# Performance work log

Hardware: AMD Instinct MI355X
Metric: run time of the kernel (lower is better)

Reference implementation:

```python
import jax, jax.numpy as jnp
import numpy as np

B, S, DIM = 2, 2048, 1024
HID = 2048          # multiple_of-rounded hidden dim
E, NSH, TOPK = 8, 2, 2


def _ffn(x, w1, w2, w3):
    return (jax.nn.silu(x @ w1.T) * (x @ w3.T)) @ w2.T


def setup_inputs() -> dict:
    key = jax.random.key(0)
    ks = jax.random.split(key, 8)
    sc = 0.02  # init scale for stability
    return {
        "x": jax.random.normal(ks[0], (B, S, DIM), jnp.float32),
        "router_w": jax.random.normal(ks[1], (E, DIM), jnp.float32) * sc,
        "expert_bias": jnp.zeros((E,), jnp.float32),
        "w1": jax.random.normal(ks[2], (E, HID, DIM), jnp.float32) * sc,
        "w3": jax.random.normal(ks[3], (E, HID, DIM), jnp.float32) * sc,
        "w2": jax.random.normal(ks[4], (E, DIM, HID), jnp.float32) * sc,
        "sw1": jax.random.normal(ks[5], (NSH, HID, DIM), jnp.float32) * sc,
        "sw3": jax.random.normal(ks[6], (NSH, HID, DIM), jnp.float32) * sc,
        "sw2": jax.random.normal(ks[7], (NSH, DIM, HID), jnp.float32) * sc,
    }


def reference(x, router_w, expert_bias, w1, w3, w2, sw1, sw3, sw2):
    bs, sl, d = x.shape
    xf = x.reshape(-1, d)  # [T, d]

    # shared experts (always-on)
    shared = jnp.zeros_like(xf)
    for i in range(sw1.shape[0]):
        shared = shared + _ffn(xf, sw1[i], sw2[i], sw3[i])

    # router with aux-free load-balance bias
    logits = xf @ router_w.T + expert_bias  # [T, E]
    rw, sel = jax.lax.top_k(logits, TOPK)   # [T, K]
    rw = jax.nn.softmax(rw.astype(jnp.float32), axis=-1).astype(x.dtype)

    # combine weights per (token, expert): sum of routing weights over topk slots
    onehot = jax.nn.one_hot(sel, E, dtype=x.dtype)        # [T, K, E]
    combine = jnp.einsum('tk,tke->te', rw, onehot)        # [T, E]

    # per-expert FFN accumulated via scan (equivalent to gather-FFN-scatter)
    def body(acc, ew):
        e1, e3, e2, cw = ew  # cw: [T]
        acc = acc + cw[:, None] * _ffn(xf, e1, e2, e3)
        return acc, None

    out, _ = jax.lax.scan(body, jnp.zeros_like(xf), (w1, w3, w2, combine.T))
    out = out + shared
    return out.reshape(bs, sl, -1)
```

## Files before the change

### kernel.cpp

```cpp
#include <hip/hip_runtime.h>
#include <stdint.h>

#define T_TOK 4096
#define DIMD  1024
#define HIDN  2048
#define NEXP  8
#define RMAX  9216

typedef float f32x4 __attribute__((ext_vector_type(4)));
typedef short s16x8 __attribute__((ext_vector_type(8)));

__device__ __forceinline__ uint16_t f2bf(float f) {
    uint32_t u = __builtin_bit_cast(uint32_t, f);
    u += 0x7fffu + ((u >> 16) & 1u);
    return (uint16_t)(u >> 16);
}
__device__ __forceinline__ float bf2f(uint32_t h) {
    return __builtin_bit_cast(float, h << 16);
}
__device__ __forceinline__ uint32_t pk2(float a, float b) {
    return (uint32_t)f2bf(a) | ((uint32_t)f2bf(b) << 16);
}
__device__ __forceinline__ int swz(int r, int cbyte) {
    return r * 128 + (cbyte ^ ((r & 7) << 4));
}
__device__ __forceinline__ void gload16(const void* g, void* l) {
    __builtin_amdgcn_global_load_lds(
        (const __attribute__((address_space(1))) void*)g,
        (__attribute__((address_space(3))) void*)l, 16, 0, 0);
}
__device__ __forceinline__ void stage128x64(const uint16_t* gbase, int ldk,
                                            char* lds, int wv, int lane) {
    #pragma unroll
    for (int i = 0; i < 4; ++i) {
        int s = (wv * 4 + i) * 64 + lane;
        int row = s >> 3;
        int cb = ((s & 7) << 4) ^ ((row & 7) << 4);
        gload16(gbase + (size_t)row * ldk + (cb >> 1), lds + ((wv * 4 + i) << 10));
    }
}


__global__ void cvt_x_kernel(const float* __restrict__ x, uint16_t* __restrict__ xb) {
    int i = blockIdx.x * blockDim.x + threadIdx.x;
    float4 v = ((const float4*)x)[i];
    uint2 o; o.x = pk2(v.x, v.y); o.y = pk2(v.z, v.w);
    ((uint2*)xb)[i] = o;
}

__global__ void cvt_w_kernel(const float* __restrict__ s, uint16_t* __restrict__ d, int nquads) {
    int i = blockIdx.x * blockDim.x + threadIdx.x;
    int stride = gridDim.x * blockDim.x;
    for (; i < nquads; i += stride) {
        float4 v = ((const float4*)s)[i];
        uint2 o; o.x = pk2(v.x, v.y); o.y = pk2(v.z, v.w);
        ((uint2*)d)[i] = o;
    }
}

__global__ void router_kernel(const float* __restrict__ x, const float* __restrict__ rw,
                              const float* __restrict__ bias,
                              int* __restrict__ sel, float* __restrict__ wgt) {
    int t = blockIdx.x;
    int lane = threadIdx.x;
    int e = lane & 7, seg = lane >> 3;
    const float* xr = x + (size_t)t * DIMD + seg * 128;
    const float* wr = rw + (size_t)e * DIMD + seg * 128;
    float s = 0.f;
    #pragma unroll 8
    for (int i = 0; i < 128; ++i) s += xr[i] * wr[i];
    s += __shfl_xor(s, 8, 64);
    s += __shfl_xor(s, 16, 64);
    s += __shfl_xor(s, 32, 64);
    __shared__ float lg[8];
    if (lane < 8) lg[lane] = s + bias[lane];
    __syncthreads();
    if (lane == 0) {
        float l0 = -1e30f; int i0 = 0;
        #pragma unroll
        for (int i = 0; i < 8; ++i) { float v = lg[i]; if (v > l0) { l0 = v; i0 = i; } }
        float l1 = -1e30f; int i1 = 0;
        #pragma unroll
        for (int i = 0; i < 8; ++i) { if (i == i0) continue; float v = lg[i]; if (v > l1) { l1 = v; i1 = i; } }
        float e1 = expf(l1 - l0);
        float d = 1.f + e1;
        sel[t * 2] = i0; sel[t * 2 + 1] = i1;
        wgt[t * 2] = 1.f / d; wgt[t * 2 + 1] = e1 / d;
    }
}

__global__ void count_kernel(const int* __restrict__ sel, int* __restrict__ cnt) {
    int i = blockIdx.x * blockDim.x + threadIdx.x;
    if (i < T_TOK * 2) atomicAdd(&cnt[sel[i]], 1);
}

__global__ void offs_kernel(const int* __restrict__ cnt, int* __restrict__ offs) {
    if (threadIdx.x == 0 && blockIdx.x == 0) {
        int o = 0;
        for (int e = 0; e < NEXP; ++e) { offs[e] = o; o += (cnt[e] + 127) & ~127; }
        offs[NEXP] = o;
    }
}

__global__ void assign_kernel(const int* __restrict__ sel, const int* __restrict__ offs,
                              int* __restrict__ fill, int* __restrict__ row_of) {
    int i = blockIdx.x * blockDim.x + threadIdx.x;
    if (i < T_TOK * 2) {
        int e = sel[i];
        row_of[i] = offs[e] + atomicAdd(&fill[e], 1);
    }
}

__global__ void gather_kernel(const uint16_t* __restrict__ xb, const int* __restrict__ row_of,
                              uint16_t* __restrict__ Xg) {
    int slot = blockIdx.x;
    int pos = row_of[slot];
    int t = slot >> 1;
    const uint4* src = (const uint4*)(xb + (size_t)t * DIMD);
    uint4* dst = (uint4*)(Xg + (size_t)pos * DIMD);
    dst[threadIdx.x] = src[threadIdx.x];
}

__global__ void combine_kernel(const uint16_t* __restrict__ H2g, const int* __restrict__ row_of,
                               const float* __restrict__ wgt, float* __restrict__ out) {
    int t = blockIdx.x;
    int c = threadIdx.x * 8;
    int r0 = row_of[t * 2], r1 = row_of[t * 2 + 1];
    float w0 = wgt[t * 2], w1 = wgt[t * 2 + 1];
    uint4 a = *(const uint4*)(H2g + (size_t)r0 * DIMD + c);
    uint4 b = *(const uint4*)(H2g + (size_t)r1 * DIMD + c);
    float* o = out + (size_t)t * DIMD + c;
    o[0] += w0 * bf2f(a.x & 0xffffu) + w1 * bf2f(b.x & 0xffffu);
    o[1] += w0 * bf2f(a.x >> 16)     + w1 * bf2f(b.x >> 16);
    o[2] += w0 * bf2f(a.y & 0xffffu) + w1 * bf2f(b.y & 0xffffu);
    o[3] += w0 * bf2f(a.y >> 16)     + w1 * bf2f(b.y >> 16);
    o[4] += w0 * bf2f(a.z & 0xffffu) + w1 * bf2f(b.z & 0xffffu);
    o[5] += w0 * bf2f(a.z >> 16)     + w1 * bf2f(b.z >> 16);
    o[6] += w0 * bf2f(a.w & 0xffffu) + w1 * bf2f(b.w & 0xffffu);
    o[7] += w0 * bf2f(a.w >> 16)     + w1 * bf2f(b.w >> 16);
}


template<int ROUTED>
__global__ __launch_bounds__(256, 2)
void gemm13_kernel(const uint16_t* __restrict__ A,
                   const uint16_t* __restrict__ W1, const uint16_t* __restrict__ W3,
                   uint16_t* __restrict__ H, int ldh,
                   const int* __restrict__ offs) {
    __shared__ __align__(16) char lds[49152];
    char* As  = lds;
    char* B1s = lds + 16384;
    char* B3s = lds + 32768;

    const int K = DIMD;
    int row0 = blockIdx.x * 128;
    const uint16_t *b1 = W1, *b3 = W3;
    if (ROUTED) {
        if (row0 >= offs[NEXP]) return;
        int e = 0;
        while (row0 >= offs[e + 1]) ++e;
        size_t eo = (size_t)e * HIDN * DIMD;
        b1 += eo; b3 += eo;
    }
    int col0 = blockIdx.y * 128;

    int tid = threadIdx.x, lane = tid & 63;
    int wv = tid >> 6, wm = wv >> 1, wn = wv & 1;

    f32x4 acc1[4][4] = {};
    f32x4 acc3[4][4] = {};

    for (int kt = 0; kt < K; kt += 64) {
        __syncthreads();
        stage128x64(A  + (size_t)row0 * K + kt, K, As,  wv, lane);
        stage128x64(b1 + (size_t)col0 * K + kt, K, B1s, wv, lane);
        stage128x64(b3 + (size_t)col0 * K + kt, K, B3s, wv, lane);
        __syncthreads();

        #pragma unroll
        for (int s = 0; s < 2; ++s) {
            int cb = s * 64 + ((lane >> 4) << 4);
            s16x8 av[4];
            #pragma unroll
            for (int i = 0; i < 4; ++i)
                av[i] = *(const s16x8*)(As + swz(wm * 64 + i * 16 + (lane & 15), cb));
            #pragma unroll
            for (int j = 0; j < 4; ++j) {
                int br = wn * 64 + j * 16 + (lane & 15);
                s16x8 bv1 = *(const s16x8*)(B1s + swz(br, cb));
                s16x8 bv3 = *(const s16x8*)(B3s + swz(br, cb));
                #pragma unroll
                for (int i = 0; i < 4; ++i) {
                    acc1[i][j] = __builtin_amdgcn_mfma_f32_16x16x32_bf16(av[i], bv1, acc1[i][j], 0, 0, 0);
                    acc3[i][j] = __builtin_amdgcn_mfma_f32_16x16x32_bf16(av[i], bv3, acc3[i][j], 0, 0, 0);
                }
            }
        }
    }

    #pragma unroll
    for (int i = 0; i < 4; ++i) {
        #pragma unroll
        for (int j = 0; j < 4; ++j) {
            #pragma unroll
            for (int rg = 0; rg < 4; ++rg) {
                int row = row0 + wm * 64 + i * 16 + ((lane >> 4) << 2) + rg;
                int col = col0 + wn * 64 + j * 16 + (lane & 15);
                float a1 = acc1[i][j][rg];
                float a3 = acc3[i][j][rg];
                float hv = (a1 / (1.f + __expf(-a1))) * a3;
                H[(size_t)row * ldh + col] = f2bf(hv);
            }
        }
    }
}

template<int ROUTED>
__global__ __launch_bounds__(256, 3)
void gemm2_kernel(const uint16_t* __restrict__ A, int lda,
                  const uint16_t* __restrict__ W2, void* __restrict__ Cout,
                  const int* __restrict__ offs,
                  int K, int kSplit, long long expStride) {
    __shared__ __align__(16) char lds[32768];
    char* As = lds;
    char* Bs = lds + 16384;

    int row0 = blockIdx.x * 128;
    const uint16_t* b2 = W2;
    if (ROUTED) {
        if (row0 >= offs[NEXP]) return;
        int e = 0;
        while (row0 >= offs[e + 1]) ++e;
        b2 += (size_t)e * DIMD * HIDN;
    }
    int col0 = blockIdx.y * 128;

    int tid = threadIdx.x, lane = tid & 63;
    int wv = tid >> 6, wm = wv >> 1, wn = wv & 1;

    f32x4 acc[4][4] = {};

    for (int kt = 0; kt < K; kt += 64) {
        const uint16_t* bb = b2 + (size_t)(kt / kSplit) * expStride + (kt % kSplit);
        __syncthreads();
        stage128x64(A  + (size_t)row0 * lda + kt, lda, As, wv, lane);
        stage128x64(bb + (size_t)col0 * kSplit, kSplit, Bs, wv, lane);
        __syncthreads();

        #pragma unroll
        for (int s = 0; s < 2; ++s) {
            int cb = s * 64 + ((lane >> 4) << 4);
            s16x8 av[4];
            #pragma unroll
            for (int i = 0; i < 4; ++i)
                av[i] = *(const s16x8*)(As + swz(wm * 64 + i * 16 + (lane & 15), cb));
            #pragma unroll
            for (int j = 0; j < 4; ++j) {
                s16x8 bv = *(const s16x8*)(Bs + swz(wn * 64 + j * 16 + (lane & 15), cb));
                #pragma unroll
                for (int i = 0; i < 4; ++i)
                    acc[i][j] = __builtin_amdgcn_mfma_f32_16x16x32_bf16(av[i], bv, acc[i][j], 0, 0, 0);
            }
        }
    }

    #pragma unroll
    for (int i = 0; i < 4; ++i) {
        #pragma unroll
        for (int j = 0; j < 4; ++j) {
            #pragma unroll
            for (int rg = 0; rg < 4; ++rg) {
                int row = row0 + wm * 64 + i * 16 + ((lane >> 4) << 2) + rg;
                int col = col0 + wn * 64 + j * 16 + (lane & 15);
                float v = acc[i][j][rg];
                if (ROUTED) ((uint16_t*)Cout)[(size_t)row * DIMD + col] = f2bf(v);
                else        ((float*)Cout)[(size_t)row * DIMD + col] += v;
            }
        }
    }
}


extern "C" void kernel_launch(void* const* d_in, const int* in_sizes, int n_in,
                              void* d_out, int out_size, void* d_ws, size_t ws_size,
                              hipStream_t stream) {
    const float* x   = (const float*)d_in[0];
    const float* rw  = (const float*)d_in[1];
    const float* eb  = (const float*)d_in[2];
    const float* w1  = (const float*)d_in[3];
    const float* w3  = (const float*)d_in[4];
    const float* w2  = (const float*)d_in[5];
    const float* sw1 = (const float*)d_in[6];
    const float* sw3 = (const float*)d_in[7];
    const float* sw2 = (const float*)d_in[8];
    float* out = (float*)d_out;

    const int EW = NEXP * HIDN * DIMD;
    const int SW = 2 * HIDN * DIMD;

    char* ws = (char*)d_ws;
    size_t off = 0;
    auto alloc = [&](size_t b) { char* p = ws + off; off = (off + b + 255) & ~(size_t)255; return p; };
    uint16_t* xb  = (uint16_t*)alloc((size_t)T_TOK * DIMD * 2);
    uint16_t* Xg  = (uint16_t*)alloc((size_t)RMAX * DIMD * 2);
    uint16_t* Hg  = (uint16_t*)alloc((size_t)RMAX * HIDN * 2);
    uint16_t* H2g = (uint16_t*)alloc((size_t)RMAX * DIMD * 2);
    uint16_t* w1b = (uint16_t*)alloc((size_t)EW * 2);
    uint16_t* w3b = (uint16_t*)alloc((size_t)EW * 2);
    uint16_t* w2b = (uint16_t*)alloc((size_t)EW * 2);
    uint16_t* sw1b = (uint16_t*)alloc((size_t)SW * 2);
    uint16_t* sw3b = (uint16_t*)alloc((size_t)SW * 2);
    uint16_t* sw2b = (uint16_t*)alloc((size_t)SW * 2);
    int*   sel    = (int*)  alloc(T_TOK * 2 * 4);
    float* wgt    = (float*)alloc(T_TOK * 2 * 4);
    int*   row_of = (int*)  alloc(T_TOK * 2 * 4);
    int*   cnt    = (int*)  alloc(64);
    int*   fill   = (int*)  alloc(64);
    int*   offs   = (int*)  alloc(64);

    hipMemsetAsync(cnt, 0, 64, stream);
    hipMemsetAsync(fill, 0, 64, stream);
    hipMemsetAsync(Xg, 0, (size_t)RMAX * DIMD * 2, stream);
    hipMemsetAsync(out, 0, (size_t)out_size * sizeof(float), stream);

    cvt_w_kernel<<<2048, 256, 0, stream>>>(w1,  w1b,  EW / 4);
    cvt_w_kernel<<<2048, 256, 0, stream>>>(w3,  w3b,  EW / 4);
    cvt_w_kernel<<<2048, 256, 0, stream>>>(w2,  w2b,  EW / 4);
    cvt_w_kernel<<<1024, 256, 0, stream>>>(sw1, sw1b, SW / 4);
    cvt_w_kernel<<<1024, 256, 0, stream>>>(sw3, sw3b, SW / 4);
    cvt_w_kernel<<<1024, 256, 0, stream>>>(sw2, sw2b, SW / 4);

    cvt_x_kernel<<<4096, 256, 0, stream>>>(x, xb);
    router_kernel<<<T_TOK, 64, 0, stream>>>(x, rw, eb, sel, wgt);
    count_kernel<<<32, 256, 0, stream>>>(sel, cnt);
    offs_kernel<<<1, 1, 0, stream>>>(cnt, offs);
    assign_kernel<<<32, 256, 0, stream>>>(sel, offs, fill, row_of);
    gather_kernel<<<T_TOK * 2, 128, 0, stream>>>(xb, row_of, Xg);

    gemm13_kernel<1><<<dim3(RMAX / 128, HIDN / 128), 256, 0, stream>>>(Xg, w1b, w3b, Hg, HIDN, offs);
    gemm2_kernel<1><<<dim3(RMAX / 128, DIMD / 128), 256, 0, stream>>>(Hg, HIDN, w2b, (void*)H2g, offs,
                                                                      HIDN, HIDN, 0);
    combine_kernel<<<T_TOK, 128, 0, stream>>>(H2g, row_of, wgt, out);

    gemm13_kernel<0><<<dim3(T_TOK / 128, (2 * HIDN) / 128), 256, 0, stream>>>(xb, sw1b, sw3b, Hg, 2 * HIDN, nullptr);
    gemm2_kernel<0><<<dim3(T_TOK / 128, DIMD / 128), 256, 0, stream>>>(Hg, 2 * HIDN, sw2b, (void*)out, nullptr,
                                                                       2 * HIDN, HIDN, (long long)DIMD * HIDN);
}
```

Baseline: 503.4 us.

## Merge conversion kernels, swap GEMM grid axes, raise gemm13 occupancy bound

Replaces the seven separate fp32-to-bf16 conversion launches with a single kernel that walks all seven segments. This removes several launches and their tail effects. The GEMM grids are transposed so blockIdx.x walks output columns, meaning consecutive blocks share the same A row-tile, which should improve L2 reuse of activations and of the per-expert weights. gemm13's launch bound is raised from 2 to 3 blocks per CU, which may force register spilling given its two 4x4 accumulator sets.

```diff
diff --git a/kernel.cpp b/kernel.cpp
--- a/kernel.cpp
+++ b/kernel.cpp
@@ -41,20 +41,25 @@
 }
 
 
-__global__ void cvt_x_kernel(const float* __restrict__ x, uint16_t* __restrict__ xb) {
-    int i = blockIdx.x * blockDim.x + threadIdx.x;
-    float4 v = ((const float4*)x)[i];
-    uint2 o; o.x = pk2(v.x, v.y); o.y = pk2(v.z, v.w);
-    ((uint2*)xb)[i] = o;
-}
-
-__global__ void cvt_w_kernel(const float* __restrict__ s, uint16_t* __restrict__ d, int nquads) {
-    int i = blockIdx.x * blockDim.x + threadIdx.x;
+struct CvtArgs {
+    const float* s[7];
+    uint16_t*    d[7];
+    int          nq[7];
+};
+
+__global__ void cvt_all_kernel(CvtArgs a) {
+    int base = blockIdx.x * blockDim.x + threadIdx.x;
     int stride = gridDim.x * blockDim.x;
-    for (; i < nquads; i += stride) {
-        float4 v = ((const float4*)s)[i];
-        uint2 o; o.x = pk2(v.x, v.y); o.y = pk2(v.z, v.w);
-        ((uint2*)d)[i] = o;
+    #pragma unroll
+    for (int seg = 0; seg < 7; ++seg) {
+        const float4* sp = (const float4*)a.s[seg];
+        uint2* dp = (uint2*)a.d[seg];
+        int n = a.nq[seg];
+        for (int i = base; i < n; i += stride) {
+            float4 v = sp[i];
+            uint2 o; o.x = pk2(v.x, v.y); o.y = pk2(v.z, v.w);
+            dp[i] = o;
+        }
     }
 }
 
@@ -142,7 +147,7 @@
 
 
 template<int ROUTED>
-__global__ __launch_bounds__(256, 2)
+__global__ __launch_bounds__(256, 3)
 void gemm13_kernel(const uint16_t* __restrict__ A,
                    const uint16_t* __restrict__ W1, const uint16_t* __restrict__ W3,
                    uint16_t* __restrict__ H, int ldh,
@@ -153,7 +158,7 @@
     char* B3s = lds + 32768;
 
     const int K = DIMD;
-    int row0 = blockIdx.x * 128;
+    int row0 = blockIdx.y * 128;
     const uint16_t *b1 = W1, *b3 = W3;
     if (ROUTED) {
         if (row0 >= offs[NEXP]) return;
@@ -162,7 +167,7 @@
         size_t eo = (size_t)e * HIDN * DIMD;
         b1 += eo; b3 += eo;
     }
-    int col0 = blockIdx.y * 128;
+    int col0 = blockIdx.x * 128;
 
     int tid = threadIdx.x, lane = tid & 63;
     int wv = tid >> 6, wm = wv >> 1, wn = wv & 1;
@@ -225,7 +230,7 @@
     char* As = lds;
     char* Bs = lds + 16384;
 
-    int row0 = blockIdx.x * 128;
+    int row0 = blockIdx.y * 128;
     const uint16_t* b2 = W2;
     if (ROUTED) {
         if (row0 >= offs[NEXP]) return;
@@ -233,7 +238,7 @@
         while (row0 >= offs[e + 1]) ++e;
         b2 += (size_t)e * DIMD * HIDN;
     }
-    int col0 = blockIdx.y * 128;
+    int col0 = blockIdx.x * 128;
 
     int tid = threadIdx.x, lane = tid & 63;
     int wv = tid >> 6, wm = wv >> 1, wn = wv & 1;
@@ -323,26 +328,28 @@
     hipMemsetAsync(Xg, 0, (size_t)RMAX * DIMD * 2, stream);
     hipMemsetAsync(out, 0, (size_t)out_size * sizeof(float), stream);
 
-    cvt_w_kernel<<<2048, 256, 0, stream>>>(w1,  w1b,  EW / 4);
-    cvt_w_kernel<<<2048, 256, 0, stream>>>(w3,  w3b,  EW / 4);
-    cvt_w_kernel<<<2048, 256, 0, stream>>>(w2,  w2b,  EW / 4);
-    cvt_w_kernel<<<1024, 256, 0, stream>>>(sw1, sw1b, SW / 4);
-    cvt_w_kernel<<<1024, 256, 0, stream>>>(sw3, sw3b, SW / 4);
-    cvt_w_kernel<<<1024, 256, 0, stream>>>(sw2, sw2b, SW / 4);
-
-    cvt_x_kernel<<<4096, 256, 0, stream>>>(x, xb);
+    CvtArgs ca;
+    ca.s[0] = w1;  ca.d[0] = w1b;  ca.nq[0] = EW / 4;
+    ca.s[1] = w3;  ca.d[1] = w3b;  ca.nq[1] = EW / 4;
+    ca.s[2] = w2;  ca.d[2] = w2b;  ca.nq[2] = EW / 4;
+    ca.s[3] = sw1; ca.d[3] = sw1b; ca.nq[3] = SW / 4;
+    ca.s[4] = sw3; ca.d[4] = sw3b; ca.nq[4] = SW / 4;
+    ca.s[5] = sw2; ca.d[5] = sw2b; ca.nq[5] = SW / 4;
+    ca.s[6] = x;   ca.d[6] = xb;   ca.nq[6] = T_TOK * DIMD / 4;
+    cvt_all_kernel<<<2048, 256, 0, stream>>>(ca);
+
     router_kernel<<<T_TOK, 64, 0, stream>>>(x, rw, eb, sel, wgt);
     count_kernel<<<32, 256, 0, stream>>>(sel, cnt);
     offs_kernel<<<1, 1, 0, stream>>>(cnt, offs);
     assign_kernel<<<32, 256, 0, stream>>>(sel, offs, fill, row_of);
     gather_kernel<<<T_TOK * 2, 128, 0, stream>>>(xb, row_of, Xg);
 
-    gemm13_kernel<1><<<dim3(RMAX / 128, HIDN / 128), 256, 0, stream>>>(Xg, w1b, w3b, Hg, HIDN, offs);
-    gemm2_kernel<1><<<dim3(RMAX / 128, DIMD / 128), 256, 0, stream>>>(Hg, HIDN, w2b, (void*)H2g, offs,
+    gemm13_kernel<1><<<dim3(HIDN / 128, RMAX / 128), 256, 0, stream>>>(Xg, w1b, w3b, Hg, HIDN, offs);
+    gemm2_kernel<1><<<dim3(DIMD / 128, RMAX / 128), 256, 0, stream>>>(Hg, HIDN, w2b, (void*)H2g, offs,
                                                                       HIDN, HIDN, 0);
     combine_kernel<<<T_TOK, 128, 0, stream>>>(H2g, row_of, wgt, out);
 
-    gemm13_kernel<0><<<dim3(T_TOK / 128, (2 * HIDN) / 128), 256, 0, stream>>>(xb, sw1b, sw3b, Hg, 2 * HIDN, nullptr);
-    gemm2_kernel<0><<<dim3(T_TOK / 128, DIMD / 128), 256, 0, stream>>>(Hg, 2 * HIDN, sw2b, (void*)out, nullptr,
+    gemm13_kernel<0><<<dim3((2 * HIDN) / 128, T_TOK / 128), 256, 0, stream>>>(xb, sw1b, sw3b, Hg, 2 * HIDN, nullptr);
+    gemm2_kernel<0><<<dim3(DIMD / 128, T_TOK / 128), 256, 0, stream>>>(Hg, 2 * HIDN, sw2b, (void*)out, nullptr,
                                                                        2 * HIDN, HIDN, (long long)DIMD * HIDN);
 }
```

Result: slower. 702.8 us (+39.6%).
